# Kernel tuning notes

Measured on AMD Instinct MI355X. Metric: run time of the kernel, lower is better.

The kernel has to match this reference:

```python
import jax, jax.numpy as jnp
import numpy as np

B, S, HID, H = 2, 2048, 2048, 16
D = HID // H  # 128 head dim
SCALE = 1.0 / np.sqrt(D)


def setup_inputs() -> dict:
    key = jax.random.key(0)
    ks = jax.random.split(key, 10)
    w = lambda k, shp: (jax.random.normal(k, shp, jnp.float32) * 0.02)
    x = jax.random.normal(ks[0], (B, S, HID), jnp.float32)
    mask = jnp.tril(jnp.ones((S, S), jnp.bool_))[None, None]  # causal [1,1,S,S]
    return {
        "x": x,
        "mask": mask,
        "Wq": w(ks[1], (HID, HID)), "bq": w(ks[2], (HID,)),
        "Wk": w(ks[3], (D, HID)),   "bk": w(ks[4], (D,)),
        "Wv": w(ks[5], (D, HID)),   "bv": w(ks[6], (D,)),
        "Wo": w(ks[7], (HID, HID)), "bo": w(ks[8], (HID,)),
    }


def reference(x, mask, Wq, bq, Wk, bk, Wv, bv, Wo, bo):
    b, s, _ = x.shape
    # projections (torch Linear: x @ W.T + b)
    q = (x @ Wq.T + bq).reshape(b, s, H, D).transpose(0, 2, 1, 3)  # [B,H,S,D]
    k = x @ Wk.T + bk  # [B,S,D] single KV head
    v = x @ Wv.T + bv  # [B,S,D]
    scores = jnp.einsum("bhqd,bkd->bhqk", q, k) * SCALE  # [B,H,S,S]
    scores = jnp.where(mask, scores, -jnp.inf)
    attn = jax.nn.softmax(scores, axis=-1)
    out = jnp.einsum("bhqk,bkd->bhqd", attn, v)  # [B,H,S,D]
    out = out.transpose(0, 2, 1, 3).reshape(b, s, HID)
    return out @ Wo.T + bo
```

## Files before the change

### kernel.cpp

```cpp
#include <hip/hip_runtime.h>


#define S_LEN 2048
#define HID_  2048
#define D_    128
#define NQKV  2304

typedef __attribute__((ext_vector_type(8))) short bf16x8;
typedef __attribute__((ext_vector_type(4))) float f32x4;
typedef __attribute__((ext_vector_type(16))) float f32x16;

__device__ __forceinline__ unsigned short f2b(float f) {
  union { float f; unsigned int u; } a; a.f = f;
  unsigned int u = a.u;
  return (unsigned short)((u + 0x7fffu + ((u >> 16) & 1u)) >> 16);
}

__device__ __forceinline__ float b2f(unsigned short s) {
  union { unsigned int u; float f; } a; a.u = ((unsigned int)s) << 16;
  return a.f;
}

__device__ __forceinline__ void load_lds16(const void* g, void* l) {
  __builtin_amdgcn_global_load_lds(
      (const __attribute__((address_space(1))) void*)g,
      (__attribute__((address_space(3))) void*)l, 16, 0, 0);
}

__device__ __forceinline__ f32x4 mfma16(bf16x8 a, bf16x8 b, f32x4 c) {
  return __builtin_amdgcn_mfma_f32_16x16x32_bf16(a, b, c, 0, 0, 0);
}

__device__ __forceinline__ f32x16 mfma32(bf16x8 a, bf16x8 b, f32x16 c) {
  return __builtin_amdgcn_mfma_f32_32x32x16_bf16(a, b, c, 0, 0, 0);
}

__device__ __forceinline__ unsigned int cvtpk(float lo, float hi) {
  unsigned int r;
  asm volatile("v_cvt_pk_bf16_f32 %0, %1, %2" : "=v"(r) : "v"(lo), "v"(hi));
  return r;
}


__global__ void cast_f32_bf16_k(const float* __restrict__ in,
                                unsigned short* __restrict__ out, int n4) {
  const int idx = blockIdx.x * 256 + threadIdx.x;
  if (idx < n4) {
    const float4 v = ((const float4*)in)[idx];
    ushort4 o;
    o.x = f2b(v.x); o.y = f2b(v.y); o.z = f2b(v.z); o.w = f2b(v.w);
    ((ushort4*)out)[idx] = o;
  }
}

__global__ void build_wcat_k(const float* __restrict__ Wq,
                             const float* __restrict__ Wk,
                             const float* __restrict__ Wv,
                             const float* __restrict__ bq,
                             const float* __restrict__ bk,
                             const float* __restrict__ bv,
                             unsigned short* __restrict__ Wcat,
                             float* __restrict__ bcat,
                             float* __restrict__ Kmax) {
  const int idx = blockIdx.x * 256 + threadIdx.x;
  const int i = idx * 4;
  const int row = i >> 11;
  const int col = i & 2047;
  const float* src;
  if (row < 2048)      src = Wq + (size_t)row * 2048 + col;
  else if (row < 2176) src = Wk + (size_t)(row - 2048) * 2048 + col;
  else                 src = Wv + (size_t)(row - 2176) * 2048 + col;
  const float4 v = *(const float4*)src;
  ushort4 o;
  o.x = f2b(v.x); o.y = f2b(v.y); o.z = f2b(v.z); o.w = f2b(v.w);
  *(ushort4*)(Wcat + i) = o;
  if (idx < NQKV)
    bcat[idx] = (idx < 2048) ? bq[idx] : (idx < 2176) ? bk[idx - 2048] : bv[idx - 2176];
  if (idx < 2) Kmax[idx] = 0.f;
}

__global__ __launch_bounds__(256)
void transpose_v(const unsigned short* __restrict__ QKV,
                 unsigned short* __restrict__ Vt) {
  __shared__ unsigned short tile[64][136];
  const int tid = threadIdx.x;
  const int s0  = blockIdx.x * 64;
  const int b   = blockIdx.y;
  const int row = tid >> 2;
  const int cb  = (tid & 3) * 32;
  const unsigned short* src = QKV + (size_t)(b * S_LEN + s0 + row) * NQKV + 2176 + cb;
#pragma unroll
  for (int i = 0; i < 4; ++i)
    *(bf16x8*)&tile[row][cb + i * 8] = *(const bf16x8*)(src + i * 8);
  __syncthreads();
  const int d  = tid >> 1;
  const int sc = (tid & 1) * 32;
  unsigned short* dst = Vt + ((size_t)b * D_ + d) * S_LEN + s0 + sc;
#pragma unroll
  for (int i = 0; i < 4; ++i) {
    bf16x8 vv;
#pragma unroll
    for (int e = 0; e < 8; ++e) vv[e] = tile[sc + i * 8 + e][d];
    *(bf16x8*)(dst + i * 8) = vv;
  }
}

__global__ __launch_bounds__(256)
void kmax_k(const unsigned short* __restrict__ QKV, float* __restrict__ Kmax) {
  __shared__ float red[256];
  const int tid = threadIdx.x;
  const int b = blockIdx.x >> 3;
  const int s = (blockIdx.x & 7) * 256 + tid;
  const unsigned short* kp = QKV + (size_t)(b * S_LEN + s) * NQKV + 2048;
  float sum = 0.f;
#pragma unroll
  for (int i = 0; i < 16; ++i) {
    bf16x8 v = *(const bf16x8*)(kp + i * 8);
#pragma unroll
    for (int e = 0; e < 8; ++e) { const float f = b2f((unsigned short)v[e]); sum += f * f; }
  }
  red[tid] = sum;
  __syncthreads();
  for (int off = 128; off > 0; off >>= 1) {
    if (tid < off) red[tid] = fmaxf(red[tid], red[tid + off]);
    __syncthreads();
  }
  if (tid == 0) atomicMax((unsigned int*)(Kmax + b), __float_as_uint(red[0]));
}


template <int OUT_F32>
__global__ __launch_bounds__(256, 3)
void gemm4(const unsigned short* __restrict__ A,
           const unsigned short* __restrict__ Bm,
           const float* __restrict__ bias,
           void* __restrict__ Cv,
           int N, int K) {
  __shared__ __align__(16) char As[3][128 * 64];
  __shared__ __align__(16) char Bs[3][128 * 64];

  const int tid  = threadIdx.x;
  const int lane = tid & 63;
  const int wv   = tid >> 6;
  const int wr   = wv >> 1, wc = wv & 1;
  const int g    = lane >> 4, r = lane & 15;

  const int nwg  = gridDim.x;
  const int bid  = blockIdx.x;
  const int sbid = (bid & 7) * (nwg >> 3) + (bid >> 3);
  const int nx   = N >> 7;
  const int m0   = (sbid / nx) * 128;
  const int n0   = (sbid % nx) * 128;
  const int NT   = K >> 5;

  const size_t Kb = (size_t)K * 2;
  const char* Ab = (const char*)A + (size_t)m0 * Kb;
  const char* Bb = (const char*)Bm + (size_t)n0 * Kb;

#define STG(bufi, t)                                                           \
  {                                                                            \
    const int kb_ = (t) * 64;                                                  \
    _Pragma("unroll")                                                          \
    for (int i_ = 0; i_ < 2; ++i_) {                                           \
      const int ch_ = tid + 256 * i_;                                          \
      const int rr_ = ch_ >> 2;                                                \
      const int sl_ = (ch_ & 3) ^ (rr_ & 3);                                   \
      load_lds16(Ab + (size_t)rr_ * Kb + kb_ + sl_ * 16, As[bufi] + ch_ * 16); \
      load_lds16(Bb + (size_t)rr_ * Kb + kb_ + sl_ * 16, Bs[bufi] + ch_ * 16); \
    }                                                                          \
  }

  f32x4 acc[4][4] = {};
  const int ss = ((g ^ (r & 3)) << 4);

  STG(0, 0) STG(1, 1)
  asm volatile("s_waitcnt vmcnt(4)" ::: "memory");
  __builtin_amdgcn_s_barrier();
  __builtin_amdgcn_sched_barrier(0);

  for (int t = 0; t < NT; ++t) {
    const char* as = (const char*)As[t % 3];
    const char* bs = (const char*)Bs[t % 3];
    const bool pf = (t + 2 < NT);

    bf16x8 af[4], bfr[4];
#pragma unroll
    for (int i = 0; i < 4; ++i)
      af[i] = *(const bf16x8*)(as + (wr * 64 + i * 16 + r) * 64 + ss);
#pragma unroll
    for (int j = 0; j < 4; ++j)
      bfr[j] = *(const bf16x8*)(bs + (wc * 64 + j * 16 + r) * 64 + ss);
    if (pf) STG((t + 2) % 3, t + 2)

    asm volatile("s_waitcnt lgkmcnt(0)" ::: "memory");
    __builtin_amdgcn_sched_barrier(0);
    __builtin_amdgcn_s_setprio(1);
#pragma unroll
    for (int i = 0; i < 4; ++i)
#pragma unroll
      for (int j = 0; j < 4; ++j)
        acc[i][j] = mfma16(af[i], bfr[j], acc[i][j]);
    __builtin_amdgcn_s_setprio(0);

    if (t + 1 < NT) {
      if (pf) { asm volatile("s_waitcnt vmcnt(4)" ::: "memory"); }
      else    { asm volatile("s_waitcnt vmcnt(0)" ::: "memory"); }
      __builtin_amdgcn_s_barrier();
      __builtin_amdgcn_sched_barrier(0);
    }
  }

#pragma unroll
  for (int i = 0; i < 4; ++i) {
    const int row = m0 + wr * 64 + i * 16 + g * 4;
#pragma unroll
    for (int j = 0; j < 4; ++j) {
      const int col = n0 + wc * 64 + j * 16 + r;
      const float bb = bias[col];
#pragma unroll
      for (int e = 0; e < 4; ++e) {
        const float v = acc[i][j][e] + bb;
        if (OUT_F32) ((float*)Cv)[(size_t)(row + e) * N + col] = v;
        else ((unsigned short*)Cv)[(size_t)(row + e) * N + col] = f2b(v);
      }
    }
  }
#undef STG
}


__global__ __launch_bounds__(256, 2)
void mqa_attn(const unsigned short* __restrict__ QKV,
              const unsigned short* __restrict__ Vt,
              const float* __restrict__ Kmax,
              unsigned short* __restrict__ Ob,
              unsigned short* __restrict__ Pacc,
              float* __restrict__ Pl) {
  __shared__ __align__(16) char Ks[2][64 * 256];
  __shared__ __align__(16) char Vs[2][64 * 256];

  const int tid  = threadIdx.x;
  const int lane = tid & 63;
  const int wv   = tid >> 6;
  const int ln   = lane & 31;
  const int hi   = lane >> 5;
  const int x    = blockIdx.x;
  const int bhq  = x & 7;
  const int b    = bhq >> 2;
  const int hq   = bhq & 3;
  const int widx = x >> 3;
  int qt, t0, te, chunk;
  if (widx < 32)      { qt = 32 + widx; t0 = 0;  te = 16;         chunk = 0; }
  else if (widx < 64) { qt = 95 - widx; t0 = 16; te = qt / 2 + 1; chunk = 1; }
  else                { qt = 95 - widx; t0 = 0;  te = qt / 2 + 1; chunk = -1; }
  const int h    = hq * 4 + wv;
  const int qw   = qt * 32;
  const int lastT = qt / 2;

  bf16x8 qf[8];
  {
    const unsigned short* qp =
        QKV + (size_t)(b * S_LEN + qw + ln) * NQKV + h * D_ + hi * 8;
#pragma unroll
    for (int ch = 0; ch < 8; ++ch) qf[ch] = *(const bf16x8*)(qp + ch * 16);
  }

  const float sscale = 0.08838834764831845f * 1.4426950408889634f;
  float qn2 = 0.f;
#pragma unroll
  for (int ch = 0; ch < 8; ++ch)
#pragma unroll
    for (int e = 0; e < 8; ++e) {
      const float qv = b2f((unsigned short)qf[ch][e]);
      qn2 += qv * qv;
    }
  qn2 += __shfl_xor(qn2, 32);
  const float m0c = sqrtf(qn2) * sqrtf(Kmax[b]) * sscale + 1.0f;

  const char* kbc = (const char*)(QKV + (size_t)(b * S_LEN) * NQKV + 2048);
  const char* vbc = (const char*)(Vt + (size_t)b * D_ * S_LEN);

  f32x16 acc[4] = {};
  float accl = 0.f;

#define STAGE(bufi, t)                                                         \
  {                                                                            \
    const int kv0_ = (t) * 64;                                                 \
    _Pragma("unroll")                                                          \
    for (int i_ = 0; i_ < 4; ++i_) {                                           \
      const int ch_ = tid + 256 * i_;                                          \
      const int kr_ = ch_ >> 4;                                                \
      const int kg_ = (ch_ & 15) ^ (kr_ & 15);                                 \
      load_lds16(kbc + (size_t)(kv0_ + kr_) * (NQKV * 2) + kg_ * 16,           \
                 Ks[bufi] + ch_ * 16);                                         \
      const int vg_ = (ch_ & 15) ^ (kr_ & 15);                                 \
      const int vd_ = kr_ * 2 + (vg_ >> 3);                                    \
      load_lds16(vbc + (size_t)vd_ * (S_LEN * 2) + kv0_ * 2 + (vg_ & 7) * 16,  \
                 Vs[bufi] + ch_ * 16);                                         \
    }                                                                          \
  }

  STAGE(0, t0);
  int cur = 0;

  for (int t = t0; t < te; ++t) {
    __syncthreads();
    if (t + 1 < te) STAGE(cur ^ 1, t + 1);

    const char* ksb = Ks[cur];
    const char* vsb = Vs[cur];
    const int kv0 = t * 64;
    const bool last = (t == lastT);
    const bool doUp = (kv0 + 32 <= qw + 31);
    cur ^= 1;

    f32x16 sA = {}, sB = {};
    __builtin_amdgcn_s_setprio(1);
#pragma unroll
    for (int ch = 0; ch < 8; ++ch) {
      const int slot0 = (2 * ch + hi) ^ (ln & 15);
      const bf16x8 kf0 = *(const bf16x8*)(ksb + ln * 256 + slot0 * 16);
      sA = mfma32(kf0, qf[ch], sA);
      if (doUp) {
        const bf16x8 kf1 = *(const bf16x8*)(ksb + (32 + ln) * 256 + slot0 * 16);
        sB = mfma32(kf1, qf[ch], sB);
      }
    }
    __builtin_amdgcn_s_setprio(0);

    bf16x8 pa0, pa1, pa2, pa3;
    float p[16];

#define SOFTMAX(sv, kvtbase)                                                   \
    _Pragma("unroll")                                                          \
    for (int rr = 0; rr < 16; ++rr) {                                          \
      float e = sv[rr] * sscale - m0c;                                         \
      if (last) {                                                              \
        const int kva = (kvtbase) + (rr & 3) + 8 * (rr >> 2) + 4 * hi;         \
        e = (kva <= qw + ln) ? e : -__builtin_inff();                          \
      }                                                                        \
      const float pv_ = __builtin_amdgcn_exp2f(e);                             \
      p[rr] = pv_; accl += pv_;                                                \
    }

#define PACK2(fa, fb)                                                          \
    {                                                                          \
      const unsigned int A0 = cvtpk(p[0], p[1]),   A1 = cvtpk(p[2], p[3]);     \
      const unsigned int B0 = cvtpk(p[4], p[5]),   B1 = cvtpk(p[6], p[7]);     \
      const unsigned int C0 = cvtpk(p[8], p[9]),   C1 = cvtpk(p[10], p[11]);   \
      const unsigned int D0 = cvtpk(p[12], p[13]), D1 = cvtpk(p[14], p[15]);   \
      unsigned int X0 = hi ? A0 : B0, X1 = hi ? A1 : B1;                       \
      unsigned int Y0 = hi ? C0 : D0, Y1 = hi ? C1 : D1;                       \
      X0 = (unsigned int)__shfl_xor((int)X0, 32);                              \
      X1 = (unsigned int)__shfl_xor((int)X1, 32);                              \
      Y0 = (unsigned int)__shfl_xor((int)Y0, 32);                              \
      Y1 = (unsigned int)__shfl_xor((int)Y1, 32);                              \
      union { unsigned int w[4]; bf16x8 v; } ua, ub;                           \
      ua.w[0] = hi ? X0 : A0; ua.w[1] = hi ? X1 : A1;                          \
      ua.w[2] = hi ? B0 : X0; ua.w[3] = hi ? B1 : X1;                          \
      ub.w[0] = hi ? Y0 : C0; ub.w[1] = hi ? Y1 : C1;                          \
      ub.w[2] = hi ? D0 : Y0; ub.w[3] = hi ? D1 : Y1;                          \
      fa = ua.v; fb = ub.v;                                                    \
    }

    SOFTMAX(sA, kv0)
    PACK2(pa0, pa1)
    if (doUp) {
      SOFTMAX(sB, kv0 + 32)
      PACK2(pa2, pa3)
    }

    __builtin_amdgcn_s_setprio(1);
#pragma unroll
    for (int dt = 0; dt < 4; ++dt) {
      const int vrow = dt * 16 + (ln >> 1);
      const int gb   = (ln & 1) << 3;
      {
        const int sl = (gb + 0 + hi) ^ (vrow & 15);
        const bf16x8 vf = *(const bf16x8*)(vsb + vrow * 256 + sl * 16);
        acc[dt] = mfma32(pa0, vf, acc[dt]);
      }
      {
        const int sl = (gb + 2 + hi) ^ (vrow & 15);
        const bf16x8 vf = *(const bf16x8*)(vsb + vrow * 256 + sl * 16);
        acc[dt] = mfma32(pa1, vf, acc[dt]);
      }
      if (doUp) {
        {
          const int sl = (gb + 4 + hi) ^ (vrow & 15);
          const bf16x8 vf = *(const bf16x8*)(vsb + vrow * 256 + sl * 16);
          acc[dt] = mfma32(pa2, vf, acc[dt]);
        }
        {
          const int sl = (gb + 6 + hi) ^ (vrow & 15);
          const bf16x8 vf = *(const bf16x8*)(vsb + vrow * 256 + sl * 16);
          acc[dt] = mfma32(pa3, vf, acc[dt]);
        }
      }
    }
    __builtin_amdgcn_s_setprio(0);
#undef SOFTMAX
#undef PACK2
  }

  const float lf = accl + __shfl_xor(accl, 32);

  if (chunk < 0) {
    const float linv = 1.0f / lf;
    unsigned short* ob = Ob + (size_t)(b * S_LEN + qw) * HID_ + h * D_ + ln;
#pragma unroll
    for (int rr = 0; rr < 16; ++rr) {
      const int qr = (rr & 3) + 8 * (rr >> 2) + 4 * hi;
      const float li = __shfl(linv, qr);
#pragma unroll
      for (int dt = 0; dt < 4; ++dt)
        ob[(size_t)qr * HID_ + dt * 32] = f2b(acc[dt][rr] * li);
    }
  } else {
    const int slot = ((chunk * 2 + b) * 16 + h) * 32 + (qt - 32);
    unsigned short* pa = Pacc + (size_t)slot * 32 * 128 + ln;
#pragma unroll
    for (int rr = 0; rr < 16; ++rr) {
      const int qr = (rr & 3) + 8 * (rr >> 2) + 4 * hi;
#pragma unroll
      for (int dt = 0; dt < 4; ++dt)
        pa[qr * 128 + dt * 32] = f2b(acc[dt][rr]);
    }
    if (hi == 0) Pl[slot * 32 + ln] = lf;
  }
#undef STAGE
}

__global__ __launch_bounds__(256)
void combine_k(const unsigned short* __restrict__ Pacc,
               const float* __restrict__ Pl,
               unsigned short* __restrict__ Ob) {
  const int x  = blockIdx.x;
  const int qs = x & 31;
  const int h  = (x >> 5) & 15;
  const int b  = x >> 9;
  const int tid = threadIdx.x;
  const int q  = tid >> 3;
  const int dp = (tid & 7) * 16;
  const int s0 = (b * 16 + h) * 32 + qs;
  const int s1 = ((2 + b) * 16 + h) * 32 + qs;
  const float inv = 1.0f / (Pl[s0 * 32 + q] + Pl[s1 * 32 + q]);
  const unsigned short* a0 = Pacc + ((size_t)s0 * 32 + q) * 128 + dp;
  const unsigned short* a1 = Pacc + ((size_t)s1 * 32 + q) * 128 + dp;
  unsigned short* ob =
      Ob + (size_t)(b * S_LEN + (32 + qs) * 32 + q) * HID_ + h * D_ + dp;
  const bf16x8 v0a = *(const bf16x8*)a0, v0b = *(const bf16x8*)(a0 + 8);
  const bf16x8 v1a = *(const bf16x8*)a1, v1b = *(const bf16x8*)(a1 + 8);
  bf16x8 oa, obv;
#pragma unroll
  for (int e = 0; e < 8; ++e) {
    oa[e]  = (short)f2b((b2f((unsigned short)v0a[e]) + b2f((unsigned short)v1a[e])) * inv);
    obv[e] = (short)f2b((b2f((unsigned short)v0b[e]) + b2f((unsigned short)v1b[e])) * inv);
  }
  *(bf16x8*)ob = oa;
  *(bf16x8*)(ob + 8) = obv;
}


extern "C" void kernel_launch(void* const* d_in, const int* in_sizes, int n_in,
                              void* d_out, int out_size, void* d_ws, size_t ws_size,
                              hipStream_t stream) {
  (void)in_sizes; (void)n_in; (void)out_size; (void)ws_size;
  const float* x  = (const float*)d_in[0];
  const float* Wq = (const float*)d_in[2];
  const float* bq = (const float*)d_in[3];
  const float* Wk = (const float*)d_in[4];
  const float* bk = (const float*)d_in[5];
  const float* Wv = (const float*)d_in[6];
  const float* bv = (const float*)d_in[7];
  const float* Wo = (const float*)d_in[8];
  const float* bo = (const float*)d_in[9];
  float* out = (float*)d_out;

  char* p = (char*)d_ws;
  unsigned short* xb   = (unsigned short*)p;  p += (size_t)4096 * 2048 * 2;
  unsigned short* Wcat = (unsigned short*)p;  p += (size_t)2304 * 2048 * 2;
  float*          bcat = (float*)p;           p += 16384;
  unsigned short* Wob  = (unsigned short*)p;  p += (size_t)2048 * 2048 * 2;
  unsigned short* QKV  = (unsigned short*)p;  p += (size_t)4096 * 2304 * 2;
  unsigned short* Vt   = (unsigned short*)p;  p += (size_t)2 * 128 * 2048 * 2;
  float*          Kmax = (float*)p;           p += 64;
  unsigned short* Pacc = (unsigned short*)p;  p += (size_t)2048 * 32 * 128 * 2;
  float*          Pl   = (float*)p;           p += (size_t)2048 * 32 * 4;
  unsigned short* Ob   = xb;

  cast_f32_bf16_k<<<8192, 256, 0, stream>>>(x, xb, 2097152);
  build_wcat_k<<<4608, 256, 0, stream>>>(Wq, Wk, Wv, bq, bk, bv, Wcat, bcat, Kmax);
  cast_f32_bf16_k<<<4096, 256, 0, stream>>>(Wo, Wob, 1048576);
  gemm4<0><<<576, 256, 0, stream>>>(xb, Wcat, bcat, QKV, 2304, 2048);
  transpose_v<<<dim3(32, 2), 256, 0, stream>>>(QKV, Vt);
  kmax_k<<<16, 256, 0, stream>>>(QKV, Kmax);
  mqa_attn<<<768, 256, 0, stream>>>(QKV, Vt, Kmax, Ob, Pacc, Pl);
  combine_k<<<1024, 256, 0, stream>>>(Pacc, Pl, Ob);
  gemm4<1><<<512, 256, 0, stream>>>(Ob, Wob, bo, out, 2048, 2048);
}
```

Baseline: 181.9 us.

## Narrow QKV GEMM tile to 96 columns and compute softmax row sums via MFMA

The QKV projection GEMM is templated on column fragments per wave, and uses a 128x96 tile with 768 workgroups instead of 128x128 with 576. The aim is better balance across the CUs on 2304 output columns, with vmcnt waits adjusted for threads that issue fewer B loads. In attention, the softmax denominator is now accumulated by an extra MFMA of the probabilities against a ones vector. This replaces per-lane scalar adds and the cross-lane shuffles in the epilogue, at the cost of extra matrix instructions and another 16-register accumulator.

```diff
diff --git a/kernel.cpp b/kernel.cpp
--- a/kernel.cpp
+++ b/kernel.cpp
@@ -129,15 +129,16 @@
 }
 
 
-template <int OUT_F32>
+template <int OUT_F32, int NJ>
 __global__ __launch_bounds__(256, 3)
 void gemm4(const unsigned short* __restrict__ A,
            const unsigned short* __restrict__ Bm,
            const float* __restrict__ bias,
            void* __restrict__ Cv,
            int N, int K) {
+  constexpr int BN = 32 * NJ;
   __shared__ __align__(16) char As[3][128 * 64];
-  __shared__ __align__(16) char Bs[3][128 * 64];
+  __shared__ __align__(16) char Bs[3][BN * 64];
 
   const int tid  = threadIdx.x;
   const int lane = tid & 63;
@@ -148,9 +149,9 @@
   const int nwg  = gridDim.x;
   const int bid  = blockIdx.x;
   const int sbid = (bid & 7) * (nwg >> 3) + (bid >> 3);
-  const int nx   = N >> 7;
+  const int nx   = N / BN;
   const int m0   = (sbid / nx) * 128;
-  const int n0   = (sbid % nx) * 128;
+  const int n0   = (sbid % nx) * BN;
   const int NT   = K >> 5;
 
   const size_t Kb = (size_t)K * 2;
@@ -166,15 +167,21 @@
       const int rr_ = ch_ >> 2;                                                \
       const int sl_ = (ch_ & 3) ^ (rr_ & 3);                                   \
       load_lds16(Ab + (size_t)rr_ * Kb + kb_ + sl_ * 16, As[bufi] + ch_ * 16); \
-      load_lds16(Bb + (size_t)rr_ * Kb + kb_ + sl_ * 16, Bs[bufi] + ch_ * 16); \
+      if (NJ == 4 || ch_ < 128 * NJ)                                           \
+        load_lds16(Bb + (size_t)rr_ * Kb + kb_ + sl_ * 16, Bs[bufi] + ch_ * 16); \
     }                                                                          \
   }
-
-  f32x4 acc[4][4] = {};
+#define WAIT_TILE()                                                            \
+  {                                                                            \
+    if (NJ == 4 || tid < 128) { asm volatile("s_waitcnt vmcnt(4)" ::: "memory"); } \
+    else                      { asm volatile("s_waitcnt vmcnt(3)" ::: "memory"); } \
+  }
+
+  f32x4 acc[4][NJ] = {};
   const int ss = ((g ^ (r & 3)) << 4);
 
   STG(0, 0) STG(1, 1)
-  asm volatile("s_waitcnt vmcnt(4)" ::: "memory");
+  WAIT_TILE()
   __builtin_amdgcn_s_barrier();
   __builtin_amdgcn_sched_barrier(0);
 
@@ -183,13 +190,13 @@
     const char* bs = (const char*)Bs[t % 3];
     const bool pf = (t + 2 < NT);
 
-    bf16x8 af[4], bfr[4];
+    bf16x8 af[4], bfr[NJ];
 #pragma unroll
     for (int i = 0; i < 4; ++i)
       af[i] = *(const bf16x8*)(as + (wr * 64 + i * 16 + r) * 64 + ss);
 #pragma unroll
-    for (int j = 0; j < 4; ++j)
-      bfr[j] = *(const bf16x8*)(bs + (wc * 64 + j * 16 + r) * 64 + ss);
+    for (int j = 0; j < NJ; ++j)
+      bfr[j] = *(const bf16x8*)(bs + (wc * 16 * NJ + j * 16 + r) * 64 + ss);
     if (pf) STG((t + 2) % 3, t + 2)
 
     asm volatile("s_waitcnt lgkmcnt(0)" ::: "memory");
@@ -198,12 +205,12 @@
 #pragma unroll
     for (int i = 0; i < 4; ++i)
 #pragma unroll
-      for (int j = 0; j < 4; ++j)
+      for (int j = 0; j < NJ; ++j)
         acc[i][j] = mfma16(af[i], bfr[j], acc[i][j]);
     __builtin_amdgcn_s_setprio(0);
 
     if (t + 1 < NT) {
-      if (pf) { asm volatile("s_waitcnt vmcnt(4)" ::: "memory"); }
+      if (pf) { WAIT_TILE() }
       else    { asm volatile("s_waitcnt vmcnt(0)" ::: "memory"); }
       __builtin_amdgcn_s_barrier();
       __builtin_amdgcn_sched_barrier(0);
@@ -214,8 +221,8 @@
   for (int i = 0; i < 4; ++i) {
     const int row = m0 + wr * 64 + i * 16 + g * 4;
 #pragma unroll
-    for (int j = 0; j < 4; ++j) {
-      const int col = n0 + wc * 64 + j * 16 + r;
+    for (int j = 0; j < NJ; ++j) {
+      const int col = n0 + wc * 16 * NJ + j * 16 + r;
       const float bb = bias[col];
 #pragma unroll
       for (int e = 0; e < 4; ++e) {
@@ -226,6 +233,7 @@
     }
   }
 #undef STG
+#undef WAIT_TILE
 }
 
 
@@ -281,7 +289,10 @@
   const char* vbc = (const char*)(Vt + (size_t)b * D_ * S_LEN);
 
   f32x16 acc[4] = {};
-  float accl = 0.f;
+  f32x16 accl = {};
+  bf16x8 onesf;
+#pragma unroll
+  for (int e = 0; e < 8; ++e) onesf[e] = (short)0x3F80;
 
 #define STAGE(bufi, t)                                                         \
   {                                                                            \
@@ -339,8 +350,7 @@
         const int kva = (kvtbase) + (rr & 3) + 8 * (rr >> 2) + 4 * hi;         \
         e = (kva <= qw + ln) ? e : -__builtin_inff();                          \
       }                                                                        \
-      const float pv_ = __builtin_amdgcn_exp2f(e);                             \
-      p[rr] = pv_; accl += pv_;                                                \
+      p[rr] = __builtin_amdgcn_exp2f(e);                                       \
     }
 
 #define PACK2(fa, fb)                                                          \
@@ -371,6 +381,12 @@
     }
 
     __builtin_amdgcn_s_setprio(1);
+    accl = mfma32(pa0, onesf, accl);
+    accl = mfma32(pa1, onesf, accl);
+    if (doUp) {
+      accl = mfma32(pa2, onesf, accl);
+      accl = mfma32(pa3, onesf, accl);
+    }
 #pragma unroll
     for (int dt = 0; dt < 4; ++dt) {
       const int vrow = dt * 16 + (ln >> 1);
@@ -403,18 +419,15 @@
 #undef PACK2
   }
 
-  const float lf = accl + __shfl_xor(accl, 32);
-
   if (chunk < 0) {
-    const float linv = 1.0f / lf;
     unsigned short* ob = Ob + (size_t)(b * S_LEN + qw) * HID_ + h * D_ + ln;
 #pragma unroll
     for (int rr = 0; rr < 16; ++rr) {
       const int qr = (rr & 3) + 8 * (rr >> 2) + 4 * hi;
-      const float li = __shfl(linv, qr);
+      const float inv = 1.0f / accl[rr];
 #pragma unroll
       for (int dt = 0; dt < 4; ++dt)
-        ob[(size_t)qr * HID_ + dt * 32] = f2b(acc[dt][rr] * li);
+        ob[(size_t)qr * HID_ + dt * 32] = f2b(acc[dt][rr] * inv);
     }
   } else {
     const int slot = ((chunk * 2 + b) * 16 + h) * 32 + (qt - 32);
@@ -426,7 +439,13 @@
       for (int dt = 0; dt < 4; ++dt)
         pa[qr * 128 + dt * 32] = f2b(acc[dt][rr]);
     }
-    if (hi == 0) Pl[slot * 32 + ln] = lf;
+    if (ln == 0) {
+#pragma unroll
+      for (int rr = 0; rr < 16; ++rr) {
+        const int qr = (rr & 3) + 8 * (rr >> 2) + 4 * hi;
+        Pl[slot * 32 + qr] = accl[rr];
+      }
+    }
   }
 #undef STAGE
 }
@@ -492,10 +511,10 @@
   cast_f32_bf16_k<<<8192, 256, 0, stream>>>(x, xb, 2097152);
   build_wcat_k<<<4608, 256, 0, stream>>>(Wq, Wk, Wv, bq, bk, bv, Wcat, bcat, Kmax);
   cast_f32_bf16_k<<<4096, 256, 0, stream>>>(Wo, Wob, 1048576);
-  gemm4<0><<<576, 256, 0, stream>>>(xb, Wcat, bcat, QKV, 2304, 2048);
+  gemm4<0, 3><<<768, 256, 0, stream>>>(xb, Wcat, bcat, QKV, 2304, 2048);
   transpose_v<<<dim3(32, 2), 256, 0, stream>>>(QKV, Vt);
   kmax_k<<<16, 256, 0, stream>>>(QKV, Kmax);
   mqa_attn<<<768, 256, 0, stream>>>(QKV, Vt, Kmax, Ob, Pacc, Pl);
   combine_k<<<1024, 256, 0, stream>>>(Pacc, Pl, Ob);
-  gemm4<1><<<512, 256, 0, stream>>>(Ob, Wob, bo, out, 2048, 2048);
-}
+  gemm4<1, 4><<<512, 256, 0, stream>>>(Ob, Wob, bo, out, 2048, 2048);
+}
```

After: 181.9 us. Within noise of the previous version (+0.0%).
